# Optimization experiments

Measured on AMD Instinct MI355X. Metric: run time of the kernel, lower is better.

## Reference

```python
import jax, jax.numpy as jnp
import numpy as np

OFFSET = 1e-6   # undefined global in source; standard small constant
COS_EPS = 1e-8  # torch F.cosine_similarity default eps


def setup_inputs() -> dict:
    key = jax.random.key(0)
    B, N, M, KS = 128, 8192, 64, 3
    ks = jax.random.split(key, 7)
    memory = jax.random.normal(ks[0], (B, N, M), dtype=jnp.float32)
    k_t = jax.random.normal(ks[1], (B, M), dtype=jnp.float32)
    beta_t = jax.random.uniform(ks[2], (B,), dtype=jnp.float32) * 5.0       # key strength >= 0
    g_t = jax.random.uniform(ks[3], (B,), dtype=jnp.float32)                # gate in [0,1)
    s_t = jax.nn.softmax(jax.random.normal(ks[4], (B, KS), dtype=jnp.float32), axis=1)  # shift dist
    gamma_t = 1.0 + jax.random.uniform(ks[5], (B,), dtype=jnp.float32)      # sharpening >= 1
    w_t_minus_1 = jax.nn.softmax(jax.random.normal(ks[6], (B, N), dtype=jnp.float32), axis=1)
    return {"memory": memory, "k_t": k_t, "beta_t": beta_t, "g_t": g_t,
            "s_t": s_t, "gamma_t": gamma_t, "w_t_minus_1": w_t_minus_1}


def reference(memory, k_t, beta_t, g_t, s_t, gamma_t, w_t_minus_1):
    B, N, M = memory.shape
    # --- cosine-similarity content addressing (torch F.cosine_similarity semantics) ---
    a = memory + OFFSET                      # [B, N, M]
    b = (k_t + OFFSET)[:, None, :]           # [B, 1, M]
    num = jnp.sum(a * b, axis=-1)            # [B, N]
    denom = (jnp.maximum(jnp.linalg.norm(a, axis=-1), COS_EPS)
             * jnp.maximum(jnp.linalg.norm(b, axis=-1), COS_EPS))
    K = num / denom                          # [B, N]
    w_c = jax.nn.softmax(beta_t[:, None] * K, axis=1)
    # --- interpolation gate ---
    g = g_t[:, None]
    w_g = g * w_c + (1.0 - g) * w_t_minus_1  # [B, N]
    # w_tilde[b, i] = sum_j s[b, j] * w_g[b, (i + j - ks//2) mod N]
    ks_size = s_t.shape[1]
    c = ks_size // 2
    w_tilde = sum(s_t[:, j:j + 1] * jnp.roll(w_g, c - j, axis=1) for j in range(ks_size))
    # --- power-law sharpening ---
    w = w_tilde ** gamma_t[:, None]          # [B, N]
    # NOTE: original module returns the repeated sum (w_t_sum), not the normalized weights.
    w_sum = jnp.sum(w, axis=1, keepdims=True) + OFFSET  # [B, 1]
    return jnp.broadcast_to(w_sum, (B, N))
```

## Files before the change

### kernel.cpp

```cpp
#include <hip/hip_runtime.h>
#include <cmath>

#define NN 8192
#define MM 64
#define OFF 1e-6f
#define CEPS 1e-8f

__global__ __launch_bounds__(256) void ntm_scores(
    const float* __restrict__ memory, const float* __restrict__ k_t,
    const float* __restrict__ beta_t, float* __restrict__ out)
{
    const int blocksPerBatch = 32;
    const int rowsPerBlock = NN / blocksPerBatch;
    const int b = blockIdx.x / blocksPerBatch;
    const int rowBase = (blockIdx.x % blocksPerBatch) * rowsPerBlock;
    const int tid = threadIdx.x;
    const int lane8 = tid & 7;
    const int group = tid >> 3;

    float4 kd0 = *(const float4*)(k_t + b * MM + lane8 * 4);
    float4 kd1 = *(const float4*)(k_t + b * MM + 32 + lane8 * 4);
    kd0.x += OFF; kd0.y += OFF; kd0.z += OFF; kd0.w += OFF;
    kd1.x += OFF; kd1.y += OFF; kd1.z += OFF; kd1.w += OFF;
    float bn = kd0.x*kd0.x + kd0.y*kd0.y + kd0.z*kd0.z + kd0.w*kd0.w
             + kd1.x*kd1.x + kd1.y*kd1.y + kd1.z*kd1.z + kd1.w*kd1.w;
    #pragma unroll
    for (int m = 1; m <= 4; m <<= 1) bn += __shfl_xor(bn, m, 64);
    const float bden = fmaxf(sqrtf(bn), CEPS);
    const float beta = beta_t[b];
    const float* memb = memory + (size_t)b * NN * MM;

    #pragma unroll 2
    for (int it = 0; it < rowsPerBlock / 32; ++it) {
        const int row = rowBase + it * 32 + group;
        const float* rowp = memb + (size_t)row * MM;
        float4 a0 = *(const float4*)(rowp + lane8 * 4);
        float4 a1 = *(const float4*)(rowp + 32 + lane8 * 4);
        a0.x += OFF; a0.y += OFF; a0.z += OFF; a0.w += OFF;
        a1.x += OFF; a1.y += OFF; a1.z += OFF; a1.w += OFF;
        float num = a0.x*kd0.x + a0.y*kd0.y + a0.z*kd0.z + a0.w*kd0.w
                  + a1.x*kd1.x + a1.y*kd1.y + a1.z*kd1.z + a1.w*kd1.w;
        float nrm = a0.x*a0.x + a0.y*a0.y + a0.z*a0.z + a0.w*a0.w
                  + a1.x*a1.x + a1.y*a1.y + a1.z*a1.z + a1.w*a1.w;
        #pragma unroll
        for (int m = 1; m <= 4; m <<= 1) {
            num += __shfl_xor(num, m, 64);
            nrm += __shfl_xor(nrm, m, 64);
        }
        if (lane8 == 0) {
            const float K = num / (fmaxf(sqrtf(nrm), CEPS) * bden);
            out[(size_t)b * NN + row] = beta * K;
        }
    }
}

__device__ __forceinline__ float blockReduceSum(float x, float* red) {
    #pragma unroll
    for (int m = 32; m >= 1; m >>= 1) x += __shfl_xor(x, m, 64);
    const int wave = threadIdx.x >> 6;
    const int lane = threadIdx.x & 63;
    __syncthreads();
    if (lane == 0) red[wave] = x;
    __syncthreads();
    if (threadIdx.x < 64) {
        float y = (threadIdx.x < 16) ? red[threadIdx.x] : 0.f;
        #pragma unroll
        for (int m = 8; m >= 1; m >>= 1) y += __shfl_xor(y, m, 64);
        if (threadIdx.x == 0) red[0] = y;
    }
    __syncthreads();
    return red[0];
}

__global__ __launch_bounds__(1024) void ntm_finalize(
    const float* __restrict__ g_t, const float* __restrict__ s_t,
    const float* __restrict__ gamma_t, const float* __restrict__ w_prev,
    float* __restrict__ io)
{
    __shared__ float sh[NN];
    __shared__ float red[16];
    const int b = blockIdx.x;
    const int tid = threadIdx.x;
    const size_t base = (size_t)b * NN;

    float ev[8];
    float lsum = 0.f;
    #pragma unroll
    for (int k = 0; k < 8; ++k) {
        ev[k] = __expf(io[base + tid + k * 1024]);
        lsum += ev[k];
    }
    const float Z = blockReduceSum(lsum, red);

    const float g = g_t[b];
    const float gamma = gamma_t[b];
    const float s0 = s_t[b * 3 + 0], s1 = s_t[b * 3 + 1], s2 = s_t[b * 3 + 2];
    const float gz = g / Z;
    const float omg = 1.f - g;

    #pragma unroll
    for (int k = 0; k < 8; ++k) {
        const int i = tid + k * 1024;
        sh[i] = ev[k] * gz + omg * w_prev[base + i];
    }
    __syncthreads();

    float wsum = 0.f;
    #pragma unroll
    for (int k = 0; k < 8; ++k) {
        const int i = tid + k * 1024;
        const float wt = s0 * sh[(i + NN - 1) & (NN - 1)]
                       + s1 * sh[i]
                       + s2 * sh[(i + 1) & (NN - 1)];
        wsum += exp2f(gamma * __log2f(wt));
    }
    const float total = blockReduceSum(wsum, red) + OFF;

    #pragma unroll
    for (int k = 0; k < 8; ++k) io[base + tid + k * 1024] = total;
}

extern "C" void kernel_launch(void* const* d_in, const int* in_sizes, int n_in,
                              void* d_out, int out_size, void* d_ws, size_t ws_size,
                              hipStream_t stream) {
    const float* memory = (const float*)d_in[0];
    const float* k_t    = (const float*)d_in[1];
    const float* beta_t = (const float*)d_in[2];
    const float* g_t    = (const float*)d_in[3];
    const float* s_t    = (const float*)d_in[4];
    const float* gamma_t= (const float*)d_in[5];
    const float* w_prev = (const float*)d_in[6];
    float* out = (float*)d_out;
    const int B = in_sizes[2];

    ntm_scores<<<B * 32, 256, 0, stream>>>(memory, k_t, beta_t, out);
    ntm_finalize<<<B, 1024, 0, stream>>>(g_t, s_t, gamma_t, w_prev, out);
}
```

Measured before the change: 51.76 us.

## Fuse softmax exponent and partition sum into the scoring kernel via atomics

The scoring kernel now computes exp(beta*K) directly and accumulates each batch's softmax denominator with one atomicAdd per wavefront into workspace, zeroed by a memset. The finalize kernel loses its exp pass and its first block reduction. Memory rows are read with nontemporal vector loads, and the cosine denominator uses a reciprocal square root with beta folded into a single scale. The +1e-6 offset on memory values is dropped, which slightly changes numerics, and the extra memset launch plus atomics add some overhead.

```diff
diff --git a/kernel.cpp b/kernel.cpp
--- a/kernel.cpp
+++ b/kernel.cpp
@@ -6,14 +6,15 @@
 #define OFF 1e-6f
 #define CEPS 1e-8f
 
+typedef float float4n __attribute__((ext_vector_type(4)));
+
 __global__ __launch_bounds__(256) void ntm_scores(
     const float* __restrict__ memory, const float* __restrict__ k_t,
-    const float* __restrict__ beta_t, float* __restrict__ out)
+    const float* __restrict__ beta_t, float* __restrict__ out,
+    float* __restrict__ zacc)
 {
-    const int blocksPerBatch = 32;
-    const int rowsPerBlock = NN / blocksPerBatch;
-    const int b = blockIdx.x / blocksPerBatch;
-    const int rowBase = (blockIdx.x % blocksPerBatch) * rowsPerBlock;
+    const int b = blockIdx.x >> 5;
+    const int rowBase = (blockIdx.x & 31) * 256;
     const int tid = threadIdx.x;
     const int lane8 = tid & 7;
     const int group = tid >> 3;
@@ -27,17 +28,16 @@
     #pragma unroll
     for (int m = 1; m <= 4; m <<= 1) bn += __shfl_xor(bn, m, 64);
     const float bden = fmaxf(sqrtf(bn), CEPS);
-    const float beta = beta_t[b];
+    const float rbeta = beta_t[b] / bden;
     const float* memb = memory + (size_t)b * NN * MM;
 
-    #pragma unroll 2
-    for (int it = 0; it < rowsPerBlock / 32; ++it) {
+    float zpart = 0.f;
+    #pragma unroll
+    for (int it = 0; it < 8; ++it) {
         const int row = rowBase + it * 32 + group;
-        const float* rowp = memb + (size_t)row * MM;
-        float4 a0 = *(const float4*)(rowp + lane8 * 4);
-        float4 a1 = *(const float4*)(rowp + 32 + lane8 * 4);
-        a0.x += OFF; a0.y += OFF; a0.z += OFF; a0.w += OFF;
-        a1.x += OFF; a1.y += OFF; a1.z += OFF; a1.w += OFF;
+        const float4n* rowp = (const float4n*)(memb + (size_t)row * MM);
+        const float4n a0 = __builtin_nontemporal_load(rowp + lane8);
+        const float4n a1 = __builtin_nontemporal_load(rowp + 8 + lane8);
         float num = a0.x*kd0.x + a0.y*kd0.y + a0.z*kd0.z + a0.w*kd0.w
                   + a1.x*kd1.x + a1.y*kd1.y + a1.z*kd1.z + a1.w*kd1.w;
         float nrm = a0.x*a0.x + a0.y*a0.y + a0.z*a0.z + a0.w*a0.w
@@ -47,11 +47,14 @@
             num += __shfl_xor(num, m, 64);
             nrm += __shfl_xor(nrm, m, 64);
         }
-        if (lane8 == 0) {
-            const float K = num / (fmaxf(sqrtf(nrm), CEPS) * bden);
-            out[(size_t)b * NN + row] = beta * K;
-        }
+        const float betaK = rbeta * num * __frsqrt_rn(fmaxf(nrm, 1e-16f));
+        const float ev = __expf(betaK);
+        zpart += ev;
+        if (lane8 == 0) out[(size_t)b * NN + row] = ev;
     }
+    #pragma unroll
+    for (int m = 8; m <= 32; m <<= 1) zpart += __shfl_xor(zpart, m, 64);
+    if ((tid & 63) == 0) atomicAdd(&zacc[b], zpart);
 }
 
 __device__ __forceinline__ float blockReduceSum(float x, float* red) {
@@ -59,7 +62,6 @@
     for (int m = 32; m >= 1; m >>= 1) x += __shfl_xor(x, m, 64);
     const int wave = threadIdx.x >> 6;
     const int lane = threadIdx.x & 63;
-    __syncthreads();
     if (lane == 0) red[wave] = x;
     __syncthreads();
     if (threadIdx.x < 64) {
@@ -75,7 +77,7 @@
 __global__ __launch_bounds__(1024) void ntm_finalize(
     const float* __restrict__ g_t, const float* __restrict__ s_t,
     const float* __restrict__ gamma_t, const float* __restrict__ w_prev,
-    float* __restrict__ io)
+    const float* __restrict__ zacc, float* __restrict__ io)
 {
     __shared__ float sh[NN];
     __shared__ float red[16];
@@ -83,15 +85,7 @@
     const int tid = threadIdx.x;
     const size_t base = (size_t)b * NN;
 
-    float ev[8];
-    float lsum = 0.f;
-    #pragma unroll
-    for (int k = 0; k < 8; ++k) {
-        ev[k] = __expf(io[base + tid + k * 1024]);
-        lsum += ev[k];
-    }
-    const float Z = blockReduceSum(lsum, red);
-
+    const float Z = zacc[b];
     const float g = g_t[b];
     const float gamma = gamma_t[b];
     const float s0 = s_t[b * 3 + 0], s1 = s_t[b * 3 + 1], s2 = s_t[b * 3 + 2];
@@ -101,7 +95,7 @@
     #pragma unroll
     for (int k = 0; k < 8; ++k) {
         const int i = tid + k * 1024;
-        sh[i] = ev[k] * gz + omg * w_prev[base + i];
+        sh[i] = io[base + i] * gz + omg * w_prev[base + i];
     }
     __syncthreads();
 
@@ -131,8 +125,10 @@
     const float* gamma_t= (const float*)d_in[5];
     const float* w_prev = (const float*)d_in[6];
     float* out = (float*)d_out;
+    float* zacc = (float*)d_ws;
     const int B = in_sizes[2];
 
-    ntm_scores<<<B * 32, 256, 0, stream>>>(memory, k_t, beta_t, out);
-    ntm_finalize<<<B, 1024, 0, stream>>>(g_t, s_t, gamma_t, w_prev, out);
+    (void)hipMemsetAsync(zacc, 0, B * sizeof(float), stream);
+    ntm_scores<<<B * 32, 256, 0, stream>>>(memory, k_t, beta_t, out, zacc);
+    ntm_finalize<<<B, 1024, 0, stream>>>(g_t, s_t, gamma_t, w_prev, zacc, out);
 }
```

After: 108.6 us. 2.1x slower.
